# Kernel optimization log

Hardware: AMD Instinct MI355X
Metric: run time of the kernel (lower is better)

The kernel has to match this reference:

```python
import jax, jax.numpy as jnp
import numpy as np

B, S, D, H, DK, F, L, V = 4, 128, 512, 8, 64, 2048, 2, 32000
N = B * S  # nodes per side (enc and dec each)


def _pe():
    pos = np.arange(S, dtype=np.float32)[:, None]
    div = np.exp(-np.log(10000.0) * np.arange(0, D, 2, dtype=np.float32) / D)
    pe = np.zeros((S, D), dtype=np.float32)
    pe[:, 0::2] = np.sin(pos * div)
    pe[:, 1::2] = np.cos(pos * div)
    return jnp.asarray(np.tile(pe, (B, 1)))  # [N, D]


def _ln(x, g, b, eps=1e-5):
    mu = jnp.mean(x, -1, keepdims=True)
    var = jnp.mean(jnp.square(x - mu), -1, keepdims=True)
    return g * (x - mu) * jax.lax.rsqrt(var + eps) + b


def _edge_attn(q, k, v, src, dst, n_dst):
    # src_dot_dst('k','q','score') then scaled_exp, then src_mul_edge + sum scatter
    s = jnp.sum(k[src] * q[dst], -1, keepdims=True) / np.float32(np.sqrt(DK))  # [E,H,1]
    s = jnp.exp(jnp.clip(s, -10.0, 10.0))
    wv = jax.ops.segment_sum(v[src] * s, dst, num_segments=n_dst)  # [n_dst,H,DK]
    z = jax.ops.segment_sum(s, dst, num_segments=n_dst)            # [n_dst,H,1]
    return wv / z


def _attn_block(x_q, x_kv, Wq, Wk, Wv, Wo, src, dst):
    q = (x_q @ Wq).reshape(-1, H, DK)
    k = (x_kv @ Wk).reshape(-1, H, DK)
    v = (x_kv @ Wv).reshape(-1, H, DK)
    o = _edge_attn(q, k, v, src, dst, x_q.shape[0]).reshape(-1, D)
    return o @ Wo


def _forward(p, src_tok, tgt_tok, ee_src, ee_dst, dd_src, dd_dst, ed_src, ed_dst):
    (src_emb, tgt_emb, enc_Wqkv, enc_Wo, enc_ln1, enc_W1, enc_b1, enc_W2, enc_b2,
     enc_ln2, enc_lnf, dec_Wqkv, dec_Wo, dec_ln1, dec_cWq, dec_cWkv, dec_cWo,
     dec_ln2, dec_W1, dec_b1, dec_W2, dec_b2, dec_ln3, dec_lnf, gen_W, gen_b) = p
    pe = _pe()
    scale = np.float32(np.sqrt(D))
    x_e = src_emb[src_tok].reshape(N, D) * scale + pe  # token + positional embed
    x_d = tgt_emb[tgt_tok].reshape(N, D) * scale + pe
    for l in range(L):  # encoder layers (ee edges)
        xn = _ln(x_e, enc_ln1[l, 0], enc_ln1[l, 1])
        x_e = x_e + _attn_block(xn, xn, enc_Wqkv[l, 0], enc_Wqkv[l, 1], enc_Wqkv[l, 2], enc_Wo[l], ee_src, ee_dst)
        xn = _ln(x_e, enc_ln2[l, 0], enc_ln2[l, 1])
        x_e = x_e + jax.nn.relu(xn @ enc_W1[l] + enc_b1[l]) @ enc_W2[l] + enc_b2[l]
    x_e = _ln(x_e, enc_lnf[0], enc_lnf[1])
    for l in range(L):  # decoder layers: self (dd) then cross (ed)
        xn = _ln(x_d, dec_ln1[l, 0], dec_ln1[l, 1])
        x_d = x_d + _attn_block(xn, xn, dec_Wqkv[l, 0], dec_Wqkv[l, 1], dec_Wqkv[l, 2], dec_Wo[l], dd_src, dd_dst)
        xn = _ln(x_d, dec_ln2[l, 0], dec_ln2[l, 1])
        x_d = x_d + _attn_block(xn, x_e, dec_cWq[l], dec_cWkv[l, 0], dec_cWkv[l, 1], dec_cWo[l], ed_src, ed_dst)
        xn = _ln(x_d, dec_ln3[l, 0], dec_ln3[l, 1])
        x_d = x_d + jax.nn.relu(xn @ dec_W1[l] + dec_b1[l]) @ dec_W2[l] + dec_b2[l]
    x_d = _ln(x_d, dec_lnf[0], dec_lnf[1])
    return jax.nn.log_softmax(x_d @ gen_W + gen_b, axis=-1)  # generator


def setup_inputs():
    key = jax.random.key(0)
    ks = iter(jax.random.split(key, 32))
    w = lambda *shape: jax.random.normal(next(ks), shape, jnp.float32) * 0.02
    lnp = lambda n: jnp.tile(jnp.stack([jnp.ones(D), jnp.zeros(D)])[None], (n, 1, 1))
    # structured edge lists: per-sentence blocks
    i, j = np.meshgrid(np.arange(S), np.arange(S), indexing='ij')  # src pos, dst pos
    base = (np.arange(B)[:, None] * S).astype(np.int32)
    full_s = (base + i.ravel()[None, :]).ravel().astype(np.int32)
    full_d = (base + j.ravel()[None, :]).ravel().astype(np.int32)
    m = i.ravel() <= j.ravel()  # causal mask for dec self-attention
    dd_s = (base + i.ravel()[m][None, :]).ravel().astype(np.int32)
    dd_d = (base + j.ravel()[m][None, :]).ravel().astype(np.int32)
    k1, k2 = jax.random.split(next(ks))
    return dict(
        src_emb=w(V, D), tgt_emb=w(V, D),
        enc_Wqkv=w(L, 3, D, D), enc_Wo=w(L, D, D), enc_ln1=lnp(L),
        enc_W1=w(L, D, F), enc_b1=jnp.zeros((L, F)), enc_W2=w(L, F, D),
        enc_b2=jnp.zeros((L, D)), enc_ln2=lnp(L), enc_lnf=lnp(1)[0],
        dec_Wqkv=w(L, 3, D, D), dec_Wo=w(L, D, D), dec_ln1=lnp(L),
        dec_cWq=w(L, D, D), dec_cWkv=w(L, 2, D, D), dec_cWo=w(L, D, D), dec_ln2=lnp(L),
        dec_W1=w(L, D, F), dec_b1=jnp.zeros((L, F)), dec_W2=w(L, F, D),
        dec_b2=jnp.zeros((L, D)), dec_ln3=lnp(L), dec_lnf=lnp(1)[0],
        gen_W=w(D, V), gen_b=jnp.zeros((V,)),
        src_tok=jax.random.randint(k1, (B, S), 0, V, jnp.int32),
        tgt_tok=jax.random.randint(k2, (B, S), 0, V, jnp.int32),
        ee_src=jnp.asarray(full_s), ee_dst=jnp.asarray(full_d),
        dd_src=jnp.asarray(dd_s), dd_dst=jnp.asarray(dd_d),
        ed_src=jnp.asarray(full_s), ed_dst=jnp.asarray(full_d),
    )


def reference(src_emb, tgt_emb, enc_Wqkv, enc_Wo, enc_ln1, enc_W1, enc_b1, enc_W2,
              enc_b2, enc_ln2, enc_lnf, dec_Wqkv, dec_Wo, dec_ln1, dec_cWq,
              dec_cWkv, dec_cWo, dec_ln2, dec_W1, dec_b1, dec_W2, dec_b2,
              dec_ln3, dec_lnf, gen_W, gen_b, src_tok, tgt_tok, ee_src, ee_dst,
              dd_src, dd_dst, ed_src, ed_dst):
    p = (src_emb, tgt_emb, enc_Wqkv, enc_Wo, enc_ln1, enc_W1, enc_b1, enc_W2,
         enc_b2, enc_ln2, enc_lnf, dec_Wqkv, dec_Wo, dec_ln1, dec_cWq, dec_cWkv,
         dec_cWo, dec_ln2, dec_W1, dec_b1, dec_W2, dec_b2, dec_ln3, dec_lnf,
         gen_W, gen_b)
    return _forward(p, src_tok, tgt_tok, ee_src, ee_dst, dd_src, dd_dst, ed_src, ed_dst)
```

## Files before the change

kernel.cpp:

```cpp
#include <hip/hip_runtime.h>
#include <cstddef>

constexpr int cB = 4, cS = 128, cD = 512, cH = 8, cDK = 64, cF = 2048, cL = 2, cV = 32000;
constexpr int cN = cB * cS;

typedef __attribute__((ext_vector_type(8)))  short short8;
typedef __attribute__((ext_vector_type(4)))  float f32x4;
typedef __attribute__((ext_vector_type(16))) float f32x16;

__device__ __forceinline__ short f2bf(float x) {
    unsigned u = __builtin_bit_cast(unsigned, x);
    unsigned r = (u + 0x7fffu + ((u >> 16) & 1u)) >> 16;
    return (short)r;
}
__device__ __forceinline__ short f2h(float x) {
    return __builtin_bit_cast(short, (_Float16)x);
}
__device__ __forceinline__ float h2f(short s) {
    return (float)__builtin_bit_cast(_Float16, s);
}

__device__ __forceinline__ void bar_lgkm() {
    asm volatile("s_waitcnt lgkmcnt(0)" ::: "memory");
    __builtin_amdgcn_s_barrier();
    asm volatile("" ::: "memory");
}

__global__ __launch_bounds__(256) void embed_k(const float* __restrict__ e0,
                                               const int* __restrict__ t0,
                                               float* __restrict__ X0,
                                               const float* __restrict__ e1,
                                               const int* __restrict__ t1,
                                               float* __restrict__ X1)
{
    const float* emb = blockIdx.z ? e1 : e0;
    const int* tok   = blockIdx.z ? t1 : t0;
    float* X         = blockIdx.z ? X1 : X0;
    int n = blockIdx.x;
    int tid = threadIdx.x;
    int t = tok[n];
    int pos = n & (cS - 1);
    const float scale = 22.62741699796952f;
    for (int d = tid; d < cD; d += 256) {
        int i2 = d & ~1;
        float div = expf(-9.210340371976184f * (float)i2 / (float)cD);
        float arg = (float)pos * div;
        float p = (d & 1) ? cosf(arg) : sinf(arg);
        X[(long)n * cD + d] = emb[(long)t * cD + d] * scale + p;
    }
}

__global__ __launch_bounds__(256) void ln_k(const float* __restrict__ X,
                                            const float* __restrict__ g,
                                            const float* __restrict__ bta,
                                            short* __restrict__ Yb)
{
    __shared__ float red[256];
    int row = blockIdx.x, tid = threadIdx.x;
    const float* x = X + (long)row * cD;
    float v0 = x[tid], v1 = x[tid + 256];

    red[tid] = v0 + v1;
    __syncthreads();
    for (int st = 128; st > 0; st >>= 1) { if (tid < st) red[tid] += red[tid + st]; __syncthreads(); }
    float mu = red[0] * (1.0f / (float)cD);
    __syncthreads();

    float d0 = v0 - mu, d1 = v1 - mu;
    red[tid] = d0 * d0 + d1 * d1;
    __syncthreads();
    for (int st = 128; st > 0; st >>= 1) { if (tid < st) red[tid] += red[tid + st]; __syncthreads(); }
    float var = red[0] * (1.0f / (float)cD);
    float rs = rsqrtf(var + 1e-5f);

    Yb[(long)row * cD + tid]       = f2bf(g[tid]       * d0 * rs + bta[tid]);
    Yb[(long)row * cD + tid + 256] = f2bf(g[tid + 256] * d1 * rs + bta[tid + 256]);
}

struct TCP { const float* s[24]; };

__global__ __launch_bounds__(256) void tconv_k(TCP ptrs, short* __restrict__ dst,
                                               int K, int N)
{
    __shared__ float t[64][65];
    const float* s = ptrs.s[blockIdx.z];
    short* d = dst + (long)blockIdx.z * K * N;
    int k0 = blockIdx.y * 64, n0 = blockIdx.x * 64;
    int tid = threadIdx.x;
    const f32x4* s4 = (const f32x4*)s;
#pragma unroll
    for (int i = 0; i < 4; i++) {
        int lin = tid + i * 256;
        int r = lin >> 4, c4 = lin & 15;
        f32x4 v = s4[(long)(k0 + r) * (N >> 2) + (n0 >> 2) + c4];
        t[r][c4 * 4 + 0] = v[0]; t[r][c4 * 4 + 1] = v[1];
        t[r][c4 * 4 + 2] = v[2]; t[r][c4 * 4 + 3] = v[3];
    }
    __syncthreads();
#pragma unroll
    for (int i = 0; i < 2; i++) {
        int lin = tid + i * 256;
        int r = lin >> 3, c8 = lin & 7;
        short8 o;
#pragma unroll
        for (int j = 0; j < 8; j++) o[j] = f2bf(t[c8 * 8 + j][r]);
        *(short8*)&d[(long)(n0 + r) * K + k0 + c8 * 8] = o;
    }
}

template <int MR, int NR, bool LNF>
__global__ __launch_bounds__(512) void gemm8_k(
    const short* __restrict__ Abf, const float* __restrict__ Af,
    const float* __restrict__ lng, const float* __restrict__ lnb,
    const short* __restrict__ Bt,
    const float* __restrict__ bias, const float* __restrict__ res,
    float* __restrict__ C, short* __restrict__ Cb,
    int N, int K, int relu, long btStride, long cStride)
{
    constexpr int BM = MR * 32, BN = NR * 32, PITCH = 136;
    constexpr int ACH = (BM * 128) / (8 * 512);
    constexpr int BCH = (BN * 128) / (8 * 512);
    static_assert(ACH >= 1 && BCH >= 1, "tile too small");
    __shared__ short As[2][BM * PITCH];
    __shared__ short Bs[2][BN * PITCH];
    __shared__ float red[4][64][MR * NR * 4];
    __shared__ float mu_s[BM], rs_s[BM];
    __shared__ float gb_s[2][LNF ? 512 : 8];

    const short* Bm = Bt + (long)blockIdx.z * btStride;
    int tid = threadIdx.x;
    int lane = tid & 63, wid = tid >> 6;
    int grp = wid >> 2, quad = wid & 3;
    int wr = quad >> 1, wc = quad & 1;
    int m0 = blockIdx.y * BM, n0 = blockIdx.x * BN;
    int lrow = lane & 15, koff = (lane >> 4) * 8;
    const int Kh = K >> 1;

    if constexpr (LNF) {
        constexpr int TPR = 512 / BM;
        int r = tid / TPR, sub = tid % TPR;
        const f32x4* row4 = (const f32x4*)(Af + (long)(m0 + r) * K);
        float s = 0.f, s2 = 0.f;
        for (int i = sub; i < (K >> 2); i += TPR) {
            f32x4 v = row4[i];
            s  += v[0] + v[1] + v[2] + v[3];
            s2 += v[0] * v[0] + v[1] * v[1] + v[2] * v[2] + v[3] * v[3];
        }
#pragma unroll
        for (int o = TPR >> 1; o > 0; o >>= 1) {
            s += __shfl_xor(s, o); s2 += __shfl_xor(s2, o);
        }
        if (sub == 0) {
            float mu = s / (float)K;
            float var = s2 / (float)K - mu * mu;
            mu_s[r] = mu; rs_s[r] = rsqrtf(var + 1e-5f);
        }
        if (tid < 512) { gb_s[0][tid] = lng[tid]; gb_s[1][tid] = lnb[tid]; }
        bar_lgkm();
    }

    f32x4 acc[MR][NR];
#pragma unroll
    for (int m = 0; m < MR; m++)
#pragma unroll
        for (int n = 0; n < NR; n++) acc[m][n] = f32x4{0.f, 0.f, 0.f, 0.f};

    short8 qa0[ACH], qa1[ACH], qb0[BCH], qb1[BCH];

    auto stage = [&](int step, short8 (&qa)[ACH], short8 (&qb)[BCH]) {
#pragma unroll
        for (int i = 0; i < ACH; i++) {
            int lin = tid + i * 512, r = lin >> 4, c8 = lin & 15;
            int kg = (c8 < 8) ? (step * 64 + c8 * 8) : (Kh + step * 64 + (c8 - 8) * 8);
            if constexpr (LNF) {
                const f32x4* p = (const f32x4*)(Af + (long)(m0 + r) * K + kg);
                f32x4 f0 = p[0], f1 = p[1];
                float mu = mu_s[r], rs = rs_s[r];
                short8 o;
#pragma unroll
                for (int j = 0; j < 4; j++)
                    o[j] = f2bf((f0[j] - mu) * rs * gb_s[0][kg + j] + gb_s[1][kg + j]);
#pragma unroll
                for (int j = 0; j < 4; j++)
                    o[4 + j] = f2bf((f1[j] - mu) * rs * gb_s[0][kg + 4 + j] + gb_s[1][kg + 4 + j]);
                qa[i] = o;
            } else {
                qa[i] = *(const short8*)&Abf[(long)(m0 + r) * K + kg];
            }
        }
#pragma unroll
        for (int i = 0; i < BCH; i++) {
            int lin = tid + i * 512, r = lin >> 4, c8 = lin & 15;
            int kg = (c8 < 8) ? (step * 64 + c8 * 8) : (Kh + step * 64 + (c8 - 8) * 8);
            qb[i] = *(const short8*)&Bm[(long)(n0 + r) * K + kg];
        }
    };
    auto writeT = [&](int buf, short8 (&qa)[ACH], short8 (&qb)[BCH]) {
#pragma unroll
        for (int i = 0; i < ACH; i++) {
            int lin = tid + i * 512, r = lin >> 4, c8 = lin & 15;
            *(short8*)&As[buf][r * PITCH + c8 * 8] = qa[i];
        }
#pragma unroll
        for (int i = 0; i < BCH; i++) {
            int lin = tid + i * 512, r = lin >> 4, c8 = lin & 15;
            *(short8*)&Bs[buf][r * PITCH + c8 * 8] = qb[i];
        }
    };
    auto mfmaStep = [&](int buf) {
#pragma unroll
        for (int kk2 = 0; kk2 < 2; kk2++) {
            int kk = grp * 64 + kk2 * 32;
            short8 a[MR], b[NR];
#pragma unroll
            for (int m = 0; m < MR; m++)
                a[m] = *(const short8*)&As[buf][(wr * MR * 16 + m * 16 + lrow) * PITCH + kk + koff];
#pragma unroll
            for (int n = 0; n < NR; n++)
                b[n] = *(const short8*)&Bs[buf][(wc * NR * 16 + n * 16 + lrow) * PITCH + kk + koff];
#pragma unroll
            for (int m = 0; m < MR; m++)
#pragma unroll
                for (int n = 0; n < NR; n++)
                    acc[m][n] = __builtin_amdgcn_mfma_f32_16x16x32_bf16(a[m], b[n], acc[m][n], 0, 0, 0);
        }
    };

    const int steps = K >> 7;
    stage(0, qa0, qb0);
    if (steps > 1) stage(1, qa1, qb1);

    int st = 0;
    for (;;) {
        writeT(0, qa0, qb0);
        if (st + 2 < steps) stage(st + 2, qa0, qb0);
        bar_lgkm();
        mfmaStep(0);
        st++; if (st >= steps) break;

        writeT(1, qa1, qb1);
        if (st + 2 < steps) stage(st + 2, qa1, qb1);
        bar_lgkm();
        mfmaStep(1);
        st++; if (st >= steps) break;
    }

    __syncthreads();
    if (grp == 1) {
#pragma unroll
        for (int m = 0; m < MR; m++)
#pragma unroll
            for (int n = 0; n < NR; n++)
#pragma unroll
                for (int j = 0; j < 4; j++)
                    red[quad][lane][(m * NR + n) * 4 + j] = acc[m][n][j];
    }
    __syncthreads();
    if (grp == 0) {
#pragma unroll
        for (int m = 0; m < MR; m++) {
            int rbase = m0 + wr * MR * 16 + m * 16 + (lane >> 4) * 4;
#pragma unroll
            for (int n = 0; n < NR; n++) {
                int col = n0 + wc * NR * 16 + n * 16 + (lane & 15);
                float bv = bias ? bias[col] : 0.f;
#pragma unroll
                for (int j = 0; j < 4; j++) {
                    long row = rbase + j;
                    float v = acc[m][n][j] + red[quad][lane][(m * NR + n) * 4 + j] + bv;
                    if (res)  v += res[row * N + col];
                    if (relu) v = fmaxf(v, 0.f);
                    long off = row * N + col + (long)blockIdx.z * cStride;
                    if (C)  C[off] = v;
                    if (Cb) Cb[off] = f2bf(v);
                }
            }
        }
    }
}

__global__ __launch_bounds__(256) void attn_k(const short* __restrict__ Q,
                                              const short* __restrict__ Km,
                                              const short* __restrict__ Vm,
                                              short* __restrict__ O, int causal)
{
    __shared__ short q_s[64 * 72];
    __shared__ short k_s[128 * 72];
    __shared__ short vt_s[64 * 128];
    __shared__ short p_s[64 * 136];
    __shared__ float z_s[64];

    int tid = threadIdx.x, lane = tid & 63, wid = tid >> 6;
    int lr = lane & 15, lg = lane >> 4;
    int h = blockIdx.x, b = blockIdx.y, dstBase = blockIdx.z * 64;
    const int RS = cH * cDK;
    long qbase = ((long)b * cS + dstBase) * RS + h * cDK;
    long kbase = ((long)b * cS) * RS + h * cDK;

#pragma unroll
    for (int i = 0; i < 2; i++) {
        int lin = tid + i * 256, t = lin >> 3, c8 = lin & 7;
        *(short8*)&q_s[t * 72 + c8 * 8] = *(const short8*)&Q[qbase + (long)t * RS + c8 * 8];
    }
#pragma unroll
    for (int i = 0; i < 4; i++) {
        int lin = tid + i * 256, t = lin >> 3, c8 = lin & 7;
        *(short8*)&k_s[t * 72 + c8 * 8] = *(const short8*)&Km[kbase + (long)t * RS + c8 * 8];
    }
#pragma unroll
    for (int i = 0; i < 4; i++) {
        int lin = tid + i * 256, src = lin >> 3, c8 = lin & 7;
        short8 v = *(const short8*)&Vm[kbase + (long)src * RS + c8 * 8];
#pragma unroll
        for (int j = 0; j < 8; j++) {
            int dk = c8 * 8 + j;
            int g = (src >> 3) ^ (dk >> 3);
            vt_s[dk * 128 + g * 8 + (src & 7)] = v[j];
        }
    }
    bar_lgkm();

    f32x4 sacc[8];
#pragma unroll
    for (int n = 0; n < 8; n++) sacc[n] = f32x4{0.f, 0.f, 0.f, 0.f};
#pragma unroll
    for (int kk = 0; kk < 64; kk += 32) {
        short8 a = *(const short8*)&q_s[(wid * 16 + lr) * 72 + kk + lg * 8];
#pragma unroll
        for (int n = 0; n < 8; n++) {
            short8 bf = *(const short8*)&k_s[(n * 16 + lr) * 72 + kk + lg * 8];
            sacc[n] = __builtin_amdgcn_mfma_f32_16x16x32_bf16(a, bf, sacc[n], 0, 0, 0);
        }
    }
    float z[4] = {0.f, 0.f, 0.f, 0.f};
#pragma unroll
    for (int n = 0; n < 8; n++) {
        int src = n * 16 + lr;
#pragma unroll
        for (int j = 0; j < 4; j++) {
            int dst = dstBase + wid * 16 + lg * 4 + j;
            float s = sacc[n][j] * 0.125f;
            s = __expf(fminf(fmaxf(s, -10.f), 10.f));
            if (causal && src > dst) s = 0.f;
            sacc[n][j] = s;
            z[j] += s;
        }
    }
#pragma unroll
    for (int j = 0; j < 4; j++) {
        z[j] += __shfl_xor(z[j], 1); z[j] += __shfl_xor(z[j], 2);
        z[j] += __shfl_xor(z[j], 4); z[j] += __shfl_xor(z[j], 8);
    }
#pragma unroll
    for (int n = 0; n < 8; n++) {
        int src = n * 16 + lr;
#pragma unroll
        for (int j = 0; j < 4; j++)
            p_s[(wid * 16 + lg * 4 + j) * 136 + src] = f2bf(sacc[n][j]);
    }
    if (lr == 0) {
#pragma unroll
        for (int j = 0; j < 4; j++) z_s[wid * 16 + lg * 4 + j] = z[j];
    }
    bar_lgkm();

    f32x4 oacc[4];
#pragma unroll
    for (int n = 0; n < 4; n++) oacc[n] = f32x4{0.f, 0.f, 0.f, 0.f};
#pragma unroll
    for (int kk = 0; kk < 128; kk += 32) {
        int dkr = wid * 16 + lr;
        int g = ((kk >> 3) + lg) ^ (dkr >> 3);
        short8 a = *(const short8*)&vt_s[dkr * 128 + g * 8];
#pragma unroll
        for (int n = 0; n < 4; n++) {
            short8 bf = *(const short8*)&p_s[(n * 16 + lr) * 136 + kk + lg * 8];
            oacc[n] = __builtin_amdgcn_mfma_f32_16x16x32_bf16(a, bf, oacc[n], 0, 0, 0);
        }
    }
#pragma unroll
    for (int n = 0; n < 4; n++) {
        int dl = n * 16 + lr;
        float zz = z_s[dl];
#pragma unroll
        for (int j = 0; j < 4; j++) {
            int dk = wid * 16 + lg * 4 + j;
            O[qbase + (long)dl * RS + dk] = f2bf(oacc[n][j] / zz);
        }
    }
}

__global__ __launch_bounds__(256) void gen32_k(
    const short* __restrict__ A, const short* __restrict__ Bt,
    const float* __restrict__ bias, short* __restrict__ Ch, int N, int K)
{
    constexpr int PITCH = 40;
    constexpr int ACH = 2, BCH = 2;
    __shared__ short As[2][128 * PITCH];
    __shared__ short Bs[2][128 * PITCH];

    int bx = blockIdx.x, by = blockIdx.y;
    {
        int nb = gridDim.x * gridDim.y;
        int bid = by * gridDim.x + bx;
        int w = (bid & 7) * (nb >> 3) + (bid >> 3);
        by = w % gridDim.y; bx = w / gridDim.y;
    }
    int tid = threadIdx.x;
    int lane = tid & 63, wid = tid >> 6;
    int wr = wid >> 1, wc = wid & 1;
    int m0 = by * 128, n0 = bx * 128;
    int l31 = lane & 31, l5 = lane >> 5;

    f32x16 acc[2][2];
#pragma unroll
    for (int m = 0; m < 2; m++)
#pragma unroll
        for (int n = 0; n < 2; n++)
#pragma unroll
            for (int r = 0; r < 16; r++) acc[m][n][r] = 0.f;

    short8 qa0[ACH], qa1[ACH], qb0[BCH], qb1[BCH];
    auto stage = [&](int k0, short8 (&qa)[ACH], short8 (&qb)[BCH]) {
#pragma unroll
        for (int i = 0; i < ACH; i++) {
            int lin = tid + i * 256, r = lin >> 2, c8 = lin & 3;
            qa[i] = *(const short8*)&A[(long)(m0 + r) * K + k0 + c8 * 8];
        }
#pragma unroll
        for (int i = 0; i < BCH; i++) {
            int lin = tid + i * 256, r = lin >> 2, c8 = lin & 3;
            qb[i] = *(const short8*)&Bt[(long)(n0 + r) * K + k0 + c8 * 8];
        }
    };
    auto writeT = [&](int buf, short8 (&qa)[ACH], short8 (&qb)[BCH]) {
#pragma unroll
        for (int i = 0; i < ACH; i++) {
            int lin = tid + i * 256, r = lin >> 2, c8 = lin & 3;
            *(short8*)&As[buf][r * PITCH + c8 * 8] = qa[i];
        }
#pragma unroll
        for (int i = 0; i < BCH; i++) {
            int lin = tid + i * 256, r = lin >> 2, c8 = lin & 3;
            *(short8*)&Bs[buf][r * PITCH + c8 * 8] = qb[i];
        }
    };
    auto mfmaStep = [&](int buf) {
#pragma unroll
        for (int kk = 0; kk < 32; kk += 16) {
            short8 a[2], b[2];
#pragma unroll
            for (int m = 0; m < 2; m++)
                a[m] = *(const short8*)&As[buf][(wr * 64 + m * 32 + l31) * PITCH + kk + l5 * 8];
#pragma unroll
            for (int n = 0; n < 2; n++)
                b[n] = *(const short8*)&Bs[buf][(wc * 64 + n * 32 + l31) * PITCH + kk + l5 * 8];
#pragma unroll
            for (int m = 0; m < 2; m++)
#pragma unroll
                for (int n = 0; n < 2; n++)
                    acc[m][n] = __builtin_amdgcn_mfma_f32_32x32x16_bf16(a[m], b[n], acc[m][n], 0, 0, 0);
        }
    };

    const int steps = K >> 5;
    stage(0, qa0, qb0);
    stage(32, qa1, qb1);
    int st = 0;
    for (;;) {
        writeT(0, qa0, qb0);
        if (st + 2 < steps) stage((st + 2) * 32, qa0, qb0);
        bar_lgkm();
        mfmaStep(0);
        st++; if (st >= steps) break;

        writeT(1, qa1, qb1);
        if (st + 2 < steps) stage((st + 2) * 32, qa1, qb1);
        bar_lgkm();
        mfmaStep(1);
        st++; if (st >= steps) break;
    }

#pragma unroll
    for (int m = 0; m < 2; m++) {
#pragma unroll
        for (int n = 0; n < 2; n++) {
            int col = n0 + wc * 64 + n * 32 + l31;
            float bv = bias[col];
#pragma unroll
            for (int r = 0; r < 16; r++) {
                int row = m0 + wr * 64 + m * 32 + (r & 3) + 8 * (r >> 2) + 4 * l5;
                Ch[(long)row * N + col] = f2h(acc[m][n][r] + bv);
            }
        }
    }
}

__global__ __launch_bounds__(256) void lsm_k(const short* __restrict__ L16,
                                             float* __restrict__ Out)
{
    __shared__ float rm[256], rs[256];
    int row = blockIdx.x, tid = threadIdx.x;
    const short8* x8 = (const short8*)(L16 + (long)row * cV);
    float* o = Out + (long)row * cV;
    constexpr int NV = cV / 8;

    float m = -1e30f, s = 0.f;
    for (int i = tid; i < NV; i += 256) {
        short8 v = x8[i];
        float f[8];
#pragma unroll
        for (int j = 0; j < 8; j++) f[j] = h2f(v[j]);
        float cm = f[0];
#pragma unroll
        for (int j = 1; j < 8; j++) cm = fmaxf(cm, f[j]);
        float nm = fmaxf(m, cm);
        float a = 0.f;
#pragma unroll
        for (int j = 0; j < 8; j++) a += __expf(f[j] - nm);
        s = s * __expf(m - nm) + a;
        m = nm;
    }
    rm[tid] = m; rs[tid] = s;
    __syncthreads();
    for (int st = 128; st > 0; st >>= 1) {
        if (tid < st) {
            float m2 = rm[tid + st], s2 = rs[tid + st];
            float nm = fmaxf(rm[tid], m2);
            rs[tid] = rs[tid] * __expf(rm[tid] - nm) + s2 * __expf(m2 - nm);
            rm[tid] = nm;
        }
        __syncthreads();
    }
    float lse = rm[0] + __logf(rs[0]);

    for (int i = tid; i < NV; i += 256) {
        short8 v = x8[i];
        f32x4 o0, o1;
#pragma unroll
        for (int j = 0; j < 4; j++) o0[j] = h2f(v[j]) - lse;
#pragma unroll
        for (int j = 0; j < 4; j++) o1[j] = h2f(v[4 + j]) - lse;
        *(f32x4*)&o[i * 8]     = o0;
        *(f32x4*)&o[i * 8 + 4] = o1;
    }
}

extern "C" void kernel_launch(void* const* d_in, const int* in_sizes, int n_in,
                              void* d_out, int out_size, void* d_ws, size_t ws_size,
                              hipStream_t stream)
{
    const float* src_emb  = (const float*)d_in[0];
    const float* tgt_emb  = (const float*)d_in[1];
    const float* enc_Wqkv = (const float*)d_in[2];
    const float* enc_Wo   = (const float*)d_in[3];
    const float* enc_ln1  = (const float*)d_in[4];
    const float* enc_W1   = (const float*)d_in[5];
    const float* enc_b1   = (const float*)d_in[6];
    const float* enc_W2   = (const float*)d_in[7];
    const float* enc_b2   = (const float*)d_in[8];
    const float* enc_ln2  = (const float*)d_in[9];
    const float* enc_lnf  = (const float*)d_in[10];
    const float* dec_Wqkv = (const float*)d_in[11];
    const float* dec_Wo   = (const float*)d_in[12];
    const float* dec_ln1  = (const float*)d_in[13];
    const float* dec_cWq  = (const float*)d_in[14];
    const float* dec_cWkv = (const float*)d_in[15];
    const float* dec_cWo  = (const float*)d_in[16];
    const float* dec_ln2  = (const float*)d_in[17];
    const float* dec_W1   = (const float*)d_in[18];
    const float* dec_b1   = (const float*)d_in[19];
    const float* dec_W2   = (const float*)d_in[20];
    const float* dec_b2   = (const float*)d_in[21];
    const float* dec_ln3  = (const float*)d_in[22];
    const float* dec_lnf  = (const float*)d_in[23];
    const float* gen_W    = (const float*)d_in[24];
    const float* gen_b    = (const float*)d_in[25];
    const int* src_tok    = (const int*)d_in[26];
    const int* tgt_tok    = (const int*)d_in[27];

    const long ND = (long)cN * cD;
    const long DD = (long)cD * cD;
    const long DF = (long)cD * cF;

    float* x_e = (float*)d_ws;
    float* x_d = x_e + ND;

    short* qkvb  = (short*)(x_d + ND);
    short* ob_bf = qkvb + 3 * ND;
    short* hb_bf = ob_bf + ND;
    short* kvc   = hb_bf + (long)cN * cF;
    short* xn_bf = kvc + 4 * ND;
    short* wDD  = xn_bf + ND;
    short* wDF  = wDD + 24 * DD;
    short* wFD  = wDF + 4 * DF;
    short* genT = wFD + 4 * DF;
    short* lg16 = genT + (long)cD * cV;

    {
        TCP p{};
        int i = 0;
        for (int j = 0; j < 6; j++) p.s[i++] = enc_Wqkv + (long)j * DD;
        for (int j = 0; j < 2; j++) p.s[i++] = enc_Wo   + (long)j * DD;
        for (int j = 0; j < 6; j++) p.s[i++] = dec_Wqkv + (long)j * DD;
        for (int j = 0; j < 2; j++) p.s[i++] = dec_Wo   + (long)j * DD;
        for (int j = 0; j < 2; j++) p.s[i++] = dec_cWq  + (long)j * DD;
        for (int j = 0; j < 4; j++) p.s[i++] = dec_cWkv + (long)j * DD;
        for (int j = 0; j < 2; j++) p.s[i++] = dec_cWo  + (long)j * DD;
        tconv_k<<<dim3(cD / 64, cD / 64, 24), 256, 0, stream>>>(p, wDD, cD, cD);
    }
    {
        TCP p{};
        p.s[0] = enc_W1; p.s[1] = enc_W1 + DF; p.s[2] = dec_W1; p.s[3] = dec_W1 + DF;
        tconv_k<<<dim3(cF / 64, cD / 64, 4), 256, 0, stream>>>(p, wDF, cD, cF);
    }
    {
        TCP p{};
        p.s[0] = enc_W2; p.s[1] = enc_W2 + DF; p.s[2] = dec_W2; p.s[3] = dec_W2 + DF;
        tconv_k<<<dim3(cD / 64, cF / 64, 4), 256, 0, stream>>>(p, wFD, cF, cD);
    }
    {
        TCP p{};
        p.s[0] = gen_W;
        tconv_k<<<dim3(cV / 64, cD / 64, 1), 256, 0, stream>>>(p, genT, cD, cV);
    }

    embed_k<<<dim3(cN, 1, 2), 256, 0, stream>>>(src_emb, src_tok, x_e,
                                                tgt_emb, tgt_tok, x_d);

    dim3 gDD(cD / 32, cN / 32);
    dim3 gFFN1(cF / 64, cN / 64);
    dim3 gAttn(cH, cB, 2);

    for (int l = 0; l < cL; l++) {
        gemm8_k<1, 1, true><<<dim3(cD / 32, cN / 32, 3), 512, 0, stream>>>(
            nullptr, x_e, enc_ln1 + (long)(2 * l) * cD, enc_ln1 + (long)(2 * l + 1) * cD,
            wDD + (long)(3 * l) * DD, nullptr, nullptr, nullptr, qkvb,
            cD, cD, 0, DD, ND);
        attn_k<<<gAttn, 256, 0, stream>>>(qkvb, qkvb + ND, qkvb + 2 * ND, ob_bf, 0);
        gemm8_k<1, 1, false><<<gDD, 512, 0, stream>>>(
            ob_bf, nullptr, nullptr, nullptr, wDD + (long)(6 + l) * DD,
            nullptr, x_e, x_e, nullptr, cD, cD, 0, 0, 0);
        gemm8_k<2, 2, true><<<gFFN1, 512, 0, stream>>>(
            nullptr, x_e, enc_ln2 + (long)(2 * l) * cD, enc_ln2 + (long)(2 * l + 1) * cD,
            wDF + (long)l * DF, enc_b1 + (long)l * cF, nullptr, nullptr, hb_bf,
            cF, cD, 1, 0, 0);
        gemm8_k<1, 1, false><<<gDD, 512, 0, stream>>>(
            hb_bf, nullptr, nullptr, nullptr, wFD + (long)l * DF,
            enc_b2 + (long)l * cD, x_e, x_e, nullptr, cD, cF, 0, 0, 0);
    }

    gemm8_k<1, 1, true><<<dim3(cD / 32, cN / 32, 4), 512, 0, stream>>>(
        nullptr, x_e, enc_lnf, enc_lnf + cD,
        wDD + 18 * DD, nullptr, nullptr, nullptr, kvc, cD, cD, 0, DD, ND);

    for (int l = 0; l < cL; l++) {
        gemm8_k<1, 1, true><<<dim3(cD / 32, cN / 32, 3), 512, 0, stream>>>(
            nullptr, x_d, dec_ln1 + (long)(2 * l) * cD, dec_ln1 + (long)(2 * l + 1) * cD,
            wDD + (long)(8 + 3 * l) * DD, nullptr, nullptr, nullptr, qkvb,
            cD, cD, 0, DD, ND);
        attn_k<<<gAttn, 256, 0, stream>>>(qkvb, qkvb + ND, qkvb + 2 * ND, ob_bf, 1);
        gemm8_k<1, 1, false><<<gDD, 512, 0, stream>>>(
            ob_bf, nullptr, nullptr, nullptr, wDD + (long)(14 + l) * DD,
            nullptr, x_d, x_d, nullptr, cD, cD, 0, 0, 0);

        gemm8_k<1, 1, true><<<gDD, 512, 0, stream>>>(
            nullptr, x_d, dec_ln2 + (long)(2 * l) * cD, dec_ln2 + (long)(2 * l + 1) * cD,
            wDD + (long)(16 + l) * DD, nullptr, nullptr, nullptr, qkvb,
            cD, cD, 0, 0, 0);
        attn_k<<<gAttn, 256, 0, stream>>>(qkvb, kvc + (long)(2 * l) * ND,
                                          kvc + (long)(2 * l + 1) * ND, ob_bf, 0);
        gemm8_k<1, 1, false><<<gDD, 512, 0, stream>>>(
            ob_bf, nullptr, nullptr, nullptr, wDD + (long)(22 + l) * DD,
            nullptr, x_d, x_d, nullptr, cD, cD, 0, 0, 0);

        gemm8_k<2, 2, true><<<gFFN1, 512, 0, stream>>>(
            nullptr, x_d, dec_ln3 + (long)(2 * l) * cD, dec_ln3 + (long)(2 * l + 1) * cD,
            wDF + (long)(2 + l) * DF, dec_b1 + (long)l * cF, nullptr, nullptr, hb_bf,
            cF, cD, 1, 0, 0);
        gemm8_k<1, 1, false><<<gDD, 512, 0, stream>>>(
            hb_bf, nullptr, nullptr, nullptr, wFD + (long)(2 + l) * DF,
            dec_b2 + (long)l * cD, x_d, x_d, nullptr, cD, cF, 0, 0, 0);
    }

    ln_k<<<cN, 256, 0, stream>>>(x_d, dec_lnf, dec_lnf + cD, xn_bf);
    gen32_k<<<dim3(cV / 128, cN / 128), 256, 0, stream>>>(
        xn_bf, genT, gen_b, lg16, cV, cD);
    lsm_k<<<cN, 256, 0, stream>>>(lg16, (float*)d_out);
}
```

Baseline: 355.5 us.

## Batch encoder and decoder layer-0 self-attention; read generator weights directly in fp32

Decoder layer-0 self-attention does not depend on the encoder, so its LN+QKV GEMM, attention and output projection are merged with encoder layer 0 into single launches over a larger z grid. A per-z input/LN selector and per-stream strides make this work, and the weight conversion order is rearranged so the batched weights sit next to each other. The generator GEMM drops the separate fp32-to-bf16 transpose pass over the 512x32000 weight. It now loads fp32 weights straight into LDS and converts them to bf16 while reading MFMA operands. That adds LDS traffic and per-element conversion work inside the largest GEMM, and it moves to a single-buffered LDS scheme with extra barriers.

```diff
diff --git a/kernel.cpp b/kernel.cpp
--- a/kernel.cpp
+++ b/kernel.cpp
@@ -112,10 +112,12 @@
 __global__ __launch_bounds__(512) void gemm8_k(
     const short* __restrict__ Abf, const float* __restrict__ Af,
     const float* __restrict__ lng, const float* __restrict__ lnb,
+    const float* __restrict__ Af2, const float* __restrict__ lng2,
+    const float* __restrict__ lnb2, int zsplit,
     const short* __restrict__ Bt,
     const float* __restrict__ bias, const float* __restrict__ res,
     float* __restrict__ C, short* __restrict__ Cb,
-    int N, int K, int relu, long btStride, long cStride)
+    int N, int K, int relu, long aStride, long btStride, long cStride)
 {
     constexpr int BM = MR * 32, BN = NR * 32, PITCH = 136;
     constexpr int ACH = (BM * 128) / (8 * 512);
@@ -127,7 +129,12 @@
     __shared__ float mu_s[BM], rs_s[BM];
     __shared__ float gb_s[2][LNF ? 512 : 8];
 
-    const short* Bm = Bt + (long)blockIdx.z * btStride;
+    const int z = blockIdx.z;
+    const float* Afz = (LNF && z >= zsplit) ? Af2 : Af;
+    const float* gz  = (LNF && z >= zsplit) ? lng2 : lng;
+    const float* bz  = (LNF && z >= zsplit) ? lnb2 : lnb;
+    const short* Am = Abf ? (Abf + (long)z * aStride) : nullptr;
+    const short* Bm = Bt + (long)z * btStride;
     int tid = threadIdx.x;
     int lane = tid & 63, wid = tid >> 6;
     int grp = wid >> 2, quad = wid & 3;
@@ -139,7 +146,7 @@
     if constexpr (LNF) {
         constexpr int TPR = 512 / BM;
         int r = tid / TPR, sub = tid % TPR;
-        const f32x4* row4 = (const f32x4*)(Af + (long)(m0 + r) * K);
+        const f32x4* row4 = (const f32x4*)(Afz + (long)(m0 + r) * K);
         float s = 0.f, s2 = 0.f;
         for (int i = sub; i < (K >> 2); i += TPR) {
             f32x4 v = row4[i];
@@ -155,7 +162,7 @@
             float var = s2 / (float)K - mu * mu;
             mu_s[r] = mu; rs_s[r] = rsqrtf(var + 1e-5f);
         }
-        if (tid < 512) { gb_s[0][tid] = lng[tid]; gb_s[1][tid] = lnb[tid]; }
+        if (tid < 512) { gb_s[0][tid] = gz[tid]; gb_s[1][tid] = bz[tid]; }
         bar_lgkm();
     }
 
@@ -173,7 +180,7 @@
             int lin = tid + i * 512, r = lin >> 4, c8 = lin & 15;
             int kg = (c8 < 8) ? (step * 64 + c8 * 8) : (Kh + step * 64 + (c8 - 8) * 8);
             if constexpr (LNF) {
-                const f32x4* p = (const f32x4*)(Af + (long)(m0 + r) * K + kg);
+                const f32x4* p = (const f32x4*)(Afz + (long)(m0 + r) * K + kg);
                 f32x4 f0 = p[0], f1 = p[1];
                 float mu = mu_s[r], rs = rs_s[r];
                 short8 o;
@@ -185,7 +192,7 @@
                     o[4 + j] = f2bf((f1[j] - mu) * rs * gb_s[0][kg + 4 + j] + gb_s[1][kg + 4 + j]);
                 qa[i] = o;
             } else {
-                qa[i] = *(const short8*)&Abf[(long)(m0 + r) * K + kg];
+                qa[i] = *(const short8*)&Am[(long)(m0 + r) * K + kg];
             }
         }
 #pragma unroll
@@ -267,10 +274,10 @@
 #pragma unroll
                 for (int j = 0; j < 4; j++) {
                     long row = rbase + j;
+                    long off = row * N + col + (long)z * cStride;
                     float v = acc[m][n][j] + red[quad][lane][(m * NR + n) * 4 + j] + bv;
-                    if (res)  v += res[row * N + col];
+                    if (res)  v += res[off];
                     if (relu) v = fmaxf(v, 0.f);
-                    long off = row * N + col + (long)blockIdx.z * cStride;
                     if (C)  C[off] = v;
                     if (Cb) Cb[off] = f2bf(v);
                 }
@@ -279,10 +286,11 @@
     }
 }
 
-__global__ __launch_bounds__(256) void attn_k(const short* __restrict__ Q,
-                                              const short* __restrict__ Km,
-                                              const short* __restrict__ Vm,
-                                              short* __restrict__ O, int causal)
+__global__ __launch_bounds__(256) void attn_k(const short* __restrict__ Qb,
+                                              const short* __restrict__ Kb,
+                                              const short* __restrict__ Vb,
+                                              short* __restrict__ Ob,
+                                              int causMask, long sQKV, long sO)
 {
     __shared__ short q_s[64 * 72];
     __shared__ short k_s[128 * 72];
@@ -292,7 +300,13 @@
 
     int tid = threadIdx.x, lane = tid & 63, wid = tid >> 6;
     int lr = lane & 15, lg = lane >> 4;
-    int h = blockIdx.x, b = blockIdx.y, dstBase = blockIdx.z * 64;
+    int h = blockIdx.x, b = blockIdx.y;
+    int stream = blockIdx.z >> 1, dstBase = (blockIdx.z & 1) * 64;
+    int causal = (causMask >> stream) & 1;
+    const short* Q = Qb + (long)stream * sQKV;
+    const short* Km = Kb + (long)stream * sQKV;
+    const short* Vm = Vb + (long)stream * sQKV;
+    short* O = Ob + (long)stream * sO;
     const int RS = cH * cDK;
     long qbase = ((long)b * cS + dstBase) * RS + h * cDK;
     long kbase = ((long)b * cS) * RS + h * cDK;
@@ -391,13 +405,12 @@
 }
 
 __global__ __launch_bounds__(256) void gen32_k(
-    const short* __restrict__ A, const short* __restrict__ Bt,
+    const short* __restrict__ A, const float* __restrict__ Bw,
     const float* __restrict__ bias, short* __restrict__ Ch, int N, int K)
 {
-    constexpr int PITCH = 40;
-    constexpr int ACH = 2, BCH = 2;
-    __shared__ short As[2][128 * PITCH];
-    __shared__ short Bs[2][128 * PITCH];
+    constexpr int PA = 72, PB = 132;
+    __shared__ short As[128 * PA];
+    __shared__ float Bsf[64 * PB];
 
     int bx = blockIdx.x, by = blockIdx.y;
     {
@@ -420,41 +433,46 @@
 #pragma unroll
             for (int r = 0; r < 16; r++) acc[m][n][r] = 0.f;
 
-    short8 qa0[ACH], qa1[ACH], qb0[BCH], qb1[BCH];
-    auto stage = [&](int k0, short8 (&qa)[ACH], short8 (&qb)[BCH]) {
-#pragma unroll
-        for (int i = 0; i < ACH; i++) {
-            int lin = tid + i * 256, r = lin >> 2, c8 = lin & 3;
+    short8 qa0[4], qa1[4];
+    f32x4  qb0[8], qb1[8];
+    auto stage = [&](int k0, short8 (&qa)[4], f32x4 (&qb)[8]) {
+#pragma unroll
+        for (int i = 0; i < 4; i++) {
+            int lin = tid + i * 256, r = lin >> 3, c8 = lin & 7;
             qa[i] = *(const short8*)&A[(long)(m0 + r) * K + k0 + c8 * 8];
         }
 #pragma unroll
-        for (int i = 0; i < BCH; i++) {
-            int lin = tid + i * 256, r = lin >> 2, c8 = lin & 3;
-            qb[i] = *(const short8*)&Bt[(long)(n0 + r) * K + k0 + c8 * 8];
+        for (int i = 0; i < 8; i++) {
+            int lin = tid + i * 256, kr = lin >> 5, c4 = lin & 31;
+            qb[i] = *(const f32x4*)&Bw[(long)(k0 + kr) * N + n0 + c4 * 4];
         }
     };
-    auto writeT = [&](int buf, short8 (&qa)[ACH], short8 (&qb)[BCH]) {
-#pragma unroll
-        for (int i = 0; i < ACH; i++) {
-            int lin = tid + i * 256, r = lin >> 2, c8 = lin & 3;
-            *(short8*)&As[buf][r * PITCH + c8 * 8] = qa[i];
-        }
-#pragma unroll
-        for (int i = 0; i < BCH; i++) {
-            int lin = tid + i * 256, r = lin >> 2, c8 = lin & 3;
-            *(short8*)&Bs[buf][r * PITCH + c8 * 8] = qb[i];
+    auto writeT = [&](short8 (&qa)[4], f32x4 (&qb)[8]) {
+#pragma unroll
+        for (int i = 0; i < 4; i++) {
+            int lin = tid + i * 256, r = lin >> 3, c8 = lin & 7;
+            *(short8*)&As[r * PA + c8 * 8] = qa[i];
+        }
+#pragma unroll
+        for (int i = 0; i < 8; i++) {
+            int lin = tid + i * 256, kr = lin >> 5, c4 = lin & 31;
+            *(f32x4*)&Bsf[kr * PB + c4 * 4] = qb[i];
         }
     };
-    auto mfmaStep = [&](int buf) {
-#pragma unroll
-        for (int kk = 0; kk < 32; kk += 16) {
+    auto mfmaStep = [&]() {
+#pragma unroll
+        for (int kk = 0; kk < 64; kk += 16) {
             short8 a[2], b[2];
 #pragma unroll
             for (int m = 0; m < 2; m++)
-                a[m] = *(const short8*)&As[buf][(wr * 64 + m * 32 + l31) * PITCH + kk + l5 * 8];
-#pragma unroll
-            for (int n = 0; n < 2; n++)
-                b[n] = *(const short8*)&Bs[buf][(wc * 64 + n * 32 + l31) * PITCH + kk + l5 * 8];
+                a[m] = *(const short8*)&As[(wr * 64 + m * 32 + l31) * PA + kk + l5 * 8];
+#pragma unroll
+            for (int n = 0; n < 2; n++) {
+                int col = wc * 64 + n * 32 + l31;
+#pragma unroll
+                for (int j = 0; j < 8; j++)
+                    b[n][j] = f2bf(Bsf[(kk + l5 * 8 + j) * PB + col]);
+            }
 #pragma unroll
             for (int m = 0; m < 2; m++)
 #pragma unroll
@@ -463,21 +481,23 @@
         }
     };
 
-    const int steps = K >> 5;
+    const int steps = K >> 6;
     stage(0, qa0, qb0);
-    stage(32, qa1, qb1);
+    stage(64, qa1, qb1);
     int st = 0;
     for (;;) {
-        writeT(0, qa0, qb0);
-        if (st + 2 < steps) stage((st + 2) * 32, qa0, qb0);
+        if (st) bar_lgkm();
+        writeT(qa0, qb0);
+        if (st + 2 < steps) stage((st + 2) * 64, qa0, qb0);
         bar_lgkm();
-        mfmaStep(0);
+        mfmaStep();
         st++; if (st >= steps) break;
 
-        writeT(1, qa1, qb1);
-        if (st + 2 < steps) stage((st + 2) * 32, qa1, qb1);
         bar_lgkm();
-        mfmaStep(1);
+        writeT(qa1, qb1);
+        if (st + 2 < steps) stage((st + 2) * 64, qa1, qb1);
+        bar_lgkm();
+        mfmaStep();
         st++; if (st >= steps) break;
     }
 
@@ -586,24 +606,25 @@
     float* x_e = (float*)d_ws;
     float* x_d = x_e + ND;
 
-    short* qkvb  = (short*)(x_d + ND);
-    short* ob_bf = qkvb + 3 * ND;
-    short* hb_bf = ob_bf + ND;
+    short* qkv6  = (short*)(x_d + ND);
+    short* ob2   = qkv6 + 6 * ND;
+    short* hb_bf = ob2 + 2 * ND;
     short* kvc   = hb_bf + (long)cN * cF;
     short* xn_bf = kvc + 4 * ND;
     short* wDD  = xn_bf + ND;
     short* wDF  = wDD + 24 * DD;
     short* wFD  = wDF + 4 * DF;
-    short* genT = wFD + 4 * DF;
-    short* lg16 = genT + (long)cD * cV;
+    short* lg16 = wFD + 4 * DF;
 
     {
         TCP p{};
         int i = 0;
-        for (int j = 0; j < 6; j++) p.s[i++] = enc_Wqkv + (long)j * DD;
-        for (int j = 0; j < 2; j++) p.s[i++] = enc_Wo   + (long)j * DD;
-        for (int j = 0; j < 6; j++) p.s[i++] = dec_Wqkv + (long)j * DD;
-        for (int j = 0; j < 2; j++) p.s[i++] = dec_Wo   + (long)j * DD;
+        for (int j = 0; j < 3; j++) p.s[i++] = enc_Wqkv + (long)j * DD;
+        for (int j = 0; j < 3; j++) p.s[i++] = dec_Wqkv + (long)j * DD;
+        p.s[i++] = enc_Wo; p.s[i++] = dec_Wo;
+        for (int j = 3; j < 6; j++) p.s[i++] = enc_Wqkv + (long)j * DD;
+        for (int j = 3; j < 6; j++) p.s[i++] = dec_Wqkv + (long)j * DD;
+        p.s[i++] = enc_Wo + DD; p.s[i++] = dec_Wo + DD;
         for (int j = 0; j < 2; j++) p.s[i++] = dec_cWq  + (long)j * DD;
         for (int j = 0; j < 4; j++) p.s[i++] = dec_cWkv + (long)j * DD;
         for (int j = 0; j < 2; j++) p.s[i++] = dec_cWo  + (long)j * DD;
@@ -619,72 +640,85 @@
         p.s[0] = enc_W2; p.s[1] = enc_W2 + DF; p.s[2] = dec_W2; p.s[3] = dec_W2 + DF;
         tconv_k<<<dim3(cD / 64, cF / 64, 4), 256, 0, stream>>>(p, wFD, cF, cD);
     }
-    {
-        TCP p{};
-        p.s[0] = gen_W;
-        tconv_k<<<dim3(cV / 64, cD / 64, 1), 256, 0, stream>>>(p, genT, cD, cV);
-    }
 
     embed_k<<<dim3(cN, 1, 2), 256, 0, stream>>>(src_emb, src_tok, x_e,
                                                 tgt_emb, tgt_tok, x_d);
 
     dim3 gDD(cD / 32, cN / 32);
     dim3 gFFN1(cF / 64, cN / 64);
-    dim3 gAttn(cH, cB, 2);
+
+    gemm8_k<1, 1, true><<<dim3(cD / 32, cN / 32, 6), 512, 0, stream>>>(
+        nullptr, x_e, enc_ln1, enc_ln1 + cD,
+        x_d, dec_ln1, dec_ln1 + cD, 3,
+        wDD, nullptr, nullptr, nullptr, qkv6, cD, cD, 0, 0, DD, ND);
+    attn_k<<<dim3(cH, cB, 4), 256, 0, stream>>>(
+        qkv6, qkv6 + ND, qkv6 + 2 * ND, ob2, 0b10, 3 * ND, ND);
+    gemm8_k<1, 1, false><<<dim3(cD / 32, cN / 32, 2), 512, 0, stream>>>(
+        ob2, nullptr, nullptr, nullptr, nullptr, nullptr, nullptr, 99,
+        wDD + 6 * DD, nullptr, x_e, x_e, nullptr, cD, cD, 0, ND, DD, ND);
+
+    gemm8_k<2, 2, true><<<gFFN1, 512, 0, stream>>>(
+        nullptr, x_e, enc_ln2, enc_ln2 + cD, nullptr, nullptr, nullptr, 99,
+        wDF, enc_b1, nullptr, nullptr, hb_bf, cF, cD, 1, 0, 0, 0);
+    gemm8_k<1, 1, false><<<gDD, 512, 0, stream>>>(
+        hb_bf, nullptr, nullptr, nullptr, nullptr, nullptr, nullptr, 99,
+        wFD, enc_b2, x_e, x_e, nullptr, cD, cF, 0, 0, 0, 0);
+
+    gemm8_k<1, 1, true><<<dim3(cD / 32, cN / 32, 3), 512, 0, stream>>>(
+        nullptr, x_e, enc_ln1 + 2 * cD, enc_ln1 + 3 * cD,
+        nullptr, nullptr, nullptr, 99,
+        wDD + 8 * DD, nullptr, nullptr, nullptr, qkv6, cD, cD, 0, 0, DD, ND);
+    attn_k<<<dim3(cH, cB, 2), 256, 0, stream>>>(
+        qkv6, qkv6 + ND, qkv6 + 2 * ND, ob2, 0, 0, 0);
+    gemm8_k<1, 1, false><<<gDD, 512, 0, stream>>>(
+        ob2, nullptr, nullptr, nullptr, nullptr, nullptr, nullptr, 99,
+        wDD + 14 * DD, nullptr, x_e, x_e, nullptr, cD, cD, 0, 0, 0, 0);
+    gemm8_k<2, 2, true><<<gFFN1, 512, 0, stream>>>(
+        nullptr, x_e, enc_ln2 + 2 * cD, enc_ln2 + 3 * cD,
+        nullptr, nullptr, nullptr, 99,
+        wDF + DF, enc_b1 + cF, nullptr, nullptr, hb_bf, cF, cD, 1, 0, 0, 0);
+    gemm8_k<1, 1, false><<<gDD, 512, 0, stream>>>(
+        hb_bf, nullptr, nullptr, nullptr, nullptr, nullptr, nullptr, 99,
+        wFD + DF, enc_b2 + cD, x_e, x_e, nullptr, cD, cF, 0, 0, 0, 0);
+
+    gemm8_k<1, 1, true><<<dim3(cD / 32, cN / 32, 4), 512, 0, stream>>>(
+        nullptr, x_e, enc_lnf, enc_lnf + cD, nullptr, nullptr, nullptr, 99,
+        wDD + 18 * DD, nullptr, nullptr, nullptr, kvc, cD, cD, 0, 0, DD, ND);
 
     for (int l = 0; l < cL; l++) {
-        gemm8_k<1, 1, true><<<dim3(cD / 32, cN / 32, 3), 512, 0, stream>>>(
-            nullptr, x_e, enc_ln1 + (long)(2 * l) * cD, enc_ln1 + (long)(2 * l + 1) * cD,
-            wDD + (long)(3 * l) * DD, nullptr, nullptr, nullptr, qkvb,
-            cD, cD, 0, DD, ND);
-        attn_k<<<gAttn, 256, 0, stream>>>(qkvb, qkvb + ND, qkvb + 2 * ND, ob_bf, 0);
-        gemm8_k<1, 1, false><<<gDD, 512, 0, stream>>>(
-            ob_bf, nullptr, nullptr, nullptr, wDD + (long)(6 + l) * DD,
-            nullptr, x_e, x_e, nullptr, cD, cD, 0, 0, 0);
-        gemm8_k<2, 2, true><<<gFFN1, 512, 0, stream>>>(
-            nullptr, x_e, enc_ln2 + (long)(2 * l) * cD, enc_ln2 + (long)(2 * l + 1) * cD,
-            wDF + (long)l * DF, enc_b1 + (long)l * cF, nullptr, nullptr, hb_bf,
-            cF, cD, 1, 0, 0);
-        gemm8_k<1, 1, false><<<gDD, 512, 0, stream>>>(
-            hb_bf, nullptr, nullptr, nullptr, wFD + (long)l * DF,
-            enc_b2 + (long)l * cD, x_e, x_e, nullptr, cD, cF, 0, 0, 0);
-    }
-
-    gemm8_k<1, 1, true><<<dim3(cD / 32, cN / 32, 4), 512, 0, stream>>>(
-        nullptr, x_e, enc_lnf, enc_lnf + cD,
-        wDD + 18 * DD, nullptr, nullptr, nullptr, kvc, cD, cD, 0, DD, ND);
-
-    for (int l = 0; l < cL; l++) {
-        gemm8_k<1, 1, true><<<dim3(cD / 32, cN / 32, 3), 512, 0, stream>>>(
-            nullptr, x_d, dec_ln1 + (long)(2 * l) * cD, dec_ln1 + (long)(2 * l + 1) * cD,
-            wDD + (long)(8 + 3 * l) * DD, nullptr, nullptr, nullptr, qkvb,
-            cD, cD, 0, DD, ND);
-        attn_k<<<gAttn, 256, 0, stream>>>(qkvb, qkvb + ND, qkvb + 2 * ND, ob_bf, 1);
-        gemm8_k<1, 1, false><<<gDD, 512, 0, stream>>>(
-            ob_bf, nullptr, nullptr, nullptr, wDD + (long)(14 + l) * DD,
-            nullptr, x_d, x_d, nullptr, cD, cD, 0, 0, 0);
-
+        if (l == 1) {
+            gemm8_k<1, 1, true><<<dim3(cD / 32, cN / 32, 3), 512, 0, stream>>>(
+                nullptr, x_d, dec_ln1 + 2 * cD, dec_ln1 + 3 * cD,
+                nullptr, nullptr, nullptr, 99,
+                wDD + 11 * DD, nullptr, nullptr, nullptr, qkv6, cD, cD, 0, 0, DD, ND);
+            attn_k<<<dim3(cH, cB, 2), 256, 0, stream>>>(
+                qkv6, qkv6 + ND, qkv6 + 2 * ND, ob2, 1, 0, 0);
+            gemm8_k<1, 1, false><<<gDD, 512, 0, stream>>>(
+                ob2, nullptr, nullptr, nullptr, nullptr, nullptr, nullptr, 99,
+                wDD + 15 * DD, nullptr, x_d, x_d, nullptr, cD, cD, 0, 0, 0, 0);
+        }
         gemm8_k<1, 1, true><<<gDD, 512, 0, stream>>>(
             nullptr, x_d, dec_ln2 + (long)(2 * l) * cD, dec_ln2 + (long)(2 * l + 1) * cD,
-            wDD + (long)(16 + l) * DD, nullptr, nullptr, nullptr, qkvb,
-            cD, cD, 0, 0, 0);
-        attn_k<<<gAttn, 256, 0, stream>>>(qkvb, kvc + (long)(2 * l) * ND,
-                                          kvc + (long)(2 * l + 1) * ND, ob_bf, 0);
+            nullptr, nullptr, nullptr, 99,
+            wDD + (long)(16 + l) * DD, nullptr, nullptr, nullptr, qkv6, cD, cD, 0, 0, 0, 0);
+        attn_k<<<dim3(cH, cB, 2), 256, 0, stream>>>(
+            qkv6, kvc + (long)(2 * l) * ND, kvc + (long)(2 * l + 1) * ND, ob2, 0, 0, 0);
         gemm8_k<1, 1, false><<<gDD, 512, 0, stream>>>(
-            ob_bf, nullptr, nullptr, nullptr, wDD + (long)(22 + l) * DD,
-            nullptr, x_d, x_d, nullptr, cD, cD, 0, 0, 0);
-
+            ob2, nullptr, nullptr, nullptr, nullptr, nullptr, nullptr, 99,
+            wDD + (long)(22 + l) * DD, nullptr, x_d, x_d, nullptr, cD, cD, 0, 0, 0, 0);
         gemm8_k<2, 2, true><<<gFFN1, 512, 0, stream>>>(
             nullptr, x_d, dec_ln3 + (long)(2 * l) * cD, dec_ln3 + (long)(2 * l + 1) * cD,
+            nullptr, nullptr, nullptr, 99,
             wDF + (long)(2 + l) * DF, dec_b1 + (long)l * cF, nullptr, nullptr, hb_bf,
-            cF, cD, 1, 0, 0);
+            cF, cD, 1, 0, 0, 0);
         gemm8_k<1, 1, false><<<gDD, 512, 0, stream>>>(
-            hb_bf, nullptr, nullptr, nullptr, wFD + (long)(2 + l) * DF,
-            dec_b2 + (long)l * cD, x_d, x_d, nullptr, cD, cF, 0, 0, 0);
+            hb_bf, nullptr, nullptr, nullptr, nullptr, nullptr, nullptr, 99,
+            wFD + (long)(2 + l) * DF, dec_b2 + (long)l * cD, x_d, x_d, nullptr,
+            cD, cF, 0, 0, 0, 0);
     }
 
     ln_k<<<cN, 256, 0, stream>>>(x_d, dec_lnf, dec_lnf + cD, xn_bf);
     gen32_k<<<dim3(cV / 128, cN / 128), 256, 0, stream>>>(
-        xn_bf, genT, gen_b, lg16, cV, cD);
+        xn_bf, gen_W, gen_b, lg16, cV, cD);
     lsm_k<<<cN, 256, 0, stream>>>(lg16, (float*)d_out);
 }
```

New measurement: 343.0 us. -3.5%, faster.
